# Kernel optimization log

Hardware: AMD Instinct MI355X
Metric: run time of the kernel (lower is better)

Reference implementation:

```python
import jax, jax.numpy as jnp
import numpy as np

B, T, E = 2, 2048, 1024
H = 16
D = E // H  # head_dim = 64


def setup_inputs() -> dict:
    key = jax.random.key(0)
    ks = jax.random.split(key, 9)
    s = 1.0 / np.sqrt(E)
    inp = {"x": jax.random.normal(ks[0], (B, T, E), dtype=jnp.float32)}
    # Linear params (torch nn.Linear: y = x @ W.T + b)
    inp["Wq"] = jax.random.uniform(ks[1], (E, E), jnp.float32, -s, s)
    inp["bq"] = jax.random.uniform(ks[2], (E,), jnp.float32, -s, s)
    inp["Wk"] = jax.random.uniform(ks[3], (E, E), jnp.float32, -s, s)
    inp["bk"] = jax.random.uniform(ks[4], (E,), jnp.float32, -s, s)
    inp["Wv"] = jax.random.uniform(ks[5], (E, E), jnp.float32, -s, s)
    inp["bv"] = jax.random.uniform(ks[6], (E,), jnp.float32, -s, s)
    inp["Wo"] = jax.random.uniform(ks[7], (E, E), jnp.float32, -s, s)
    inp["bo"] = jax.random.uniform(ks[8], (E,), jnp.float32, -s, s)
    return inp


def reference(x, Wq, bq, Wk, bk, Wv, bv, Wo, bo):
    # QKV projections, reshape to [B, H, T, D]
    def split_heads(y):
        return y.reshape(B, T, H, D).transpose(0, 2, 1, 3)

    Q = split_heads(x @ Wq.T + bq)
    K = split_heads(x @ Wk.T + bk)
    V = split_heads(x @ Wv.T + bv)

    scale = 1.0 / jnp.sqrt(jnp.asarray(D, x.dtype))
    scores = jnp.einsum("bhqd,bhkd->bhqk", Q, K) * scale  # [B,H,T,T]
    attn = jax.nn.softmax(scores, axis=-1)
    out = jnp.einsum("bhqk,bhkd->bhqd", attn, V)  # [B,H,T,D]
    out = out.transpose(0, 2, 1, 3).reshape(B, T, E)
    # dropout is identity in eval mode
    return out @ Wo.T + bo
```

## Files before the change

### kernel.cpp

```cpp
#include <hip/hip_runtime.h>
#include <math.h>

#define BB 2
#define TT 2048
#define EE 1024
#define HH 16
#define DD 64
#define MM (BB*TT)
#define KK EE

typedef short bf16x8 __attribute__((ext_vector_type(8)));
typedef float f32x4  __attribute__((ext_vector_type(4)));
typedef float f32x16 __attribute__((ext_vector_type(16)));
typedef unsigned int u32x4 __attribute__((ext_vector_type(4)));

__device__ __forceinline__ unsigned short f2bf(float f) {
  unsigned int u = __float_as_uint(f);
  u = (u + 0x7FFFu + ((u >> 16) & 1u)) >> 16;
  return (unsigned short)u;
}

__device__ __forceinline__ unsigned int cvtpk(float lo, float hi) {
  unsigned int r;
  asm("v_cvt_pk_bf16_f32 %0, %1, %2" : "=v"(r) : "v"(lo), "v"(hi));
  return r;
}

__device__ __forceinline__ void plswap(unsigned int &a, unsigned int &b) {
  asm("v_permlane32_swap_b32 %0, %1" : "+v"(a), "+v"(b));
}

__device__ __forceinline__ void async16(const void* g, void* l) {
  __builtin_amdgcn_global_load_lds(
      (const __attribute__((address_space(1))) unsigned int*)g,
      (__attribute__((address_space(3))) unsigned int*)l, 16, 0, 0);
}

__global__ __launch_bounds__(256) void to_bf16(
    const float* __restrict__ x,  const float* __restrict__ wq,
    const float* __restrict__ wk, const float* __restrict__ wv,
    const float* __restrict__ wo,
    unsigned short* __restrict__ xh, unsigned short* __restrict__ wcat,
    unsigned short* __restrict__ woh)
{
  int c = blockIdx.x * 256 + threadIdx.x;
  const float* src; unsigned short* dst; int off;
  if (c < 1048576) { src = x; dst = xh; off = c; }
  else {
    int r = c - 1048576;
    int w = r >> 18;
    off = r & 262143;
    if      (w == 0) { src = wq; dst = wcat; }
    else if (w == 1) { src = wk; dst = wcat + (1 << 20); }
    else if (w == 2) { src = wv; dst = wcat + (2 << 20); }
    else             { src = wo; dst = woh; }
  }
  float4 v = ((const float4*)src)[off];
  ushort4 h;
  h.x = f2bf(v.x); h.y = f2bf(v.y); h.z = f2bf(v.z); h.w = f2bf(v.w);
  ((ushort4*)dst)[off] = h;
}

template<int MODE>
__global__ __launch_bounds__(512, 6) void gemm_bf16(
    const unsigned short* __restrict__ A, const unsigned short* __restrict__ B,
    const float* __restrict__ b0p, const float* __restrict__ b1p,
    const float* __restrict__ b2p,
    unsigned short* __restrict__ oq, unsigned short* __restrict__ ok,
    unsigned short* __restrict__ ov, float* __restrict__ ofp, float qscale)
{
  constexpr int NT = (MODE == 0) ? 128 : 64;
  constexpr int JN = NT / 32;
  constexpr int BROWS = NT * 32;
  constexpr int TOT = (MODE == 0) ? 16 : 12;
  __shared__ unsigned short S[12288 + 3 * BROWS];

  const int tid  = threadIdx.x;
  const int lane = tid & 63;
  const int wv   = tid >> 6;
  const int col  = lane & 15;
  const int quad = lane >> 4;
  const int wm = (wv & 3) * 32;
  const int wn = (wv >> 2) * (NT / 2);
  const int m0 = blockIdx.x * 128;
  const int n0 = blockIdx.y * NT;

  const int srow = lane >> 2;
  const int sw16 = (((lane & 3) ^ ((lane >> 2) & 3) ^ (lane >> 4)) << 3);
  const int fswA = ((quad ^ (col & 3) ^ (col >> 2)) << 3);

  auto stage = [&](int kt, int slot) {
#pragma unroll
    for (int s = 0; s < 2; ++s) {
      const int t = wv * 2 + s;
      if (t < TOT) {
        const unsigned short* src; int rb, g0, loff;
        if (t < 8) { src = A; rb = t * 16;       g0 = m0; loff = slot * 4096; }
        else       { src = B; rb = (t - 8) * 16; g0 = n0; loff = 12288 + slot * BROWS; }
        async16(src + (size_t)(g0 + rb + srow) * KK + kt + sw16,
                S + loff + rb * 32);
      }
    }
  };

  f32x4 acc[2][JN];
  const f32x4 z = {0.f, 0.f, 0.f, 0.f};
#pragma unroll
  for (int i = 0; i < 2; ++i)
#pragma unroll
    for (int j = 0; j < JN; ++j) acc[i][j] = z;

  stage(0, 0);

#define GBODY(T, SL, S2, DOSTAGE, VMC) do {                                   \
    if (DOSTAGE) stage(((T) + 1) * 32, S2);                                   \
    asm volatile("s_waitcnt vmcnt(" #VMC ")" ::: "memory");                   \
    __builtin_amdgcn_sched_barrier(0);                                        \
    __builtin_amdgcn_s_barrier();                                             \
    __builtin_amdgcn_sched_barrier(0);                                        \
    const unsigned short* Asb = S + (SL) * 4096;                              \
    const unsigned short* Bsb = S + 12288 + (SL) * BROWS;                     \
    bf16x8 bfr[JN];                                                           \
    _Pragma("unroll")                                                         \
    for (int j = 0; j < JN; ++j)                                              \
      bfr[j] = *(const bf16x8*)(Bsb + (wn + j * 16 + col) * 32 + fswA);       \
    _Pragma("unroll")                                                         \
    for (int i = 0; i < 2; ++i) {                                             \
      bf16x8 af = *(const bf16x8*)(Asb + (wm + i * 16 + col) * 32 + fswA);    \
      _Pragma("unroll")                                                       \
      for (int j = 0; j < JN; ++j)                                            \
        acc[i][j] = __builtin_amdgcn_mfma_f32_16x16x32_bf16(af, bfr[j], acc[i][j], 0, 0, 0); \
    }                                                                         \
  } while (0)

  for (int t = 0; t < 30; t += 3) {
    GBODY(t + 0, 0, 1, 1, 2);
    GBODY(t + 1, 1, 2, 1, 2);
    GBODY(t + 2, 2, 0, 1, 2);
  }
  GBODY(30, 0, 1, 1, 2);
  GBODY(31, 1, 0, 0, 0);
#undef GBODY

  unsigned short* Cs = S;
  if (MODE == 0) {
    __syncthreads();
    const int region = n0 >> 10;
    const float* bias = (region == 0) ? b0p : (region == 1) ? b1p : b2p;
    const float scl = (region == 0) ? qscale : 1.0f;
    const int nlbase = n0 & 1023;
    const int h0 = nlbase >> 6;
    const int b = m0 >> 11, t0 = m0 & (TT - 1);
    if (region < 2) {
#pragma unroll
      for (int i = 0; i < 2; ++i)
#pragma unroll
        for (int j = 0; j < 4; ++j) {
          const int nt = wn + j * 16 + col;
          const float bs = bias[nlbase + nt];
#pragma unroll
          for (int r = 0; r < 4; ++r) {
            const int mt = wm + i * 16 + quad * 4 + r;
            Cs[mt * 136 + nt] = f2bf((acc[i][j][r] + bs) * scl);
          }
        }
      __syncthreads();
      unsigned short* dst = (region == 0) ? oq : ok;
#pragma unroll
      for (int s = 0; s < 4; ++s) {
        const int u = s * 512 + tid;
        const int mt = u >> 4, hs = (u >> 3) & 1, ch = u & 7;
        const size_t g = ((size_t)(b * HH + h0 + hs) * TT + t0 + mt) * DD + ch * 8;
        *(uint4*)(dst + g) = *(const uint4*)(Cs + mt * 136 + hs * 64 + ch * 8);
      }
    } else {
#pragma unroll
      for (int i = 0; i < 2; ++i)
#pragma unroll
        for (int j = 0; j < 4; ++j) {
          const int nt = wn + j * 16 + col;
          const float bs = bias[nlbase + nt];
          ushort4 pk;
          pk.x = f2bf(acc[i][j][0] + bs);
          pk.y = f2bf(acc[i][j][1] + bs);
          pk.z = f2bf(acc[i][j][2] + bs);
          pk.w = f2bf(acc[i][j][3] + bs);
          *(ushort4*)(Cs + nt * 136 + wm + i * 16 + quad * 4) = pk;
        }
      __syncthreads();
#pragma unroll
      for (int s = 0; s < 4; ++s) {
        const int u = s * 512 + tid;
        const int nt = u >> 4, ch = u & 15;
        const int d = nt & 63, hs = nt >> 6;
        const size_t g = ((size_t)(b * HH + h0 + hs) * DD + d) * TT + t0 + ch * 8;
        *(uint4*)(ov + g) = *(const uint4*)(Cs + nt * 136 + ch * 8);
      }
    }
  } else {
#pragma unroll
    for (int i = 0; i < 2; ++i) {
#pragma unroll
      for (int j = 0; j < JN; ++j) {
        const int n = n0 + wn + j * 16 + col;
        const float bs = b0p[n];
#pragma unroll
        for (int r = 0; r < 4; ++r) {
          const int m = m0 + wm + i * 16 + quad * 4 + r;
          ofp[(size_t)m * EE + n] = acc[i][j][r] + bs;
        }
      }
    }
  }
}

__global__ __launch_bounds__(512, 4) void flash_mfma(
    const unsigned short* __restrict__ Qb, const unsigned short* __restrict__ Kb,
    const unsigned short* __restrict__ Vtb, unsigned short* __restrict__ ctx)
{
  __shared__ unsigned short Qs[128 * 64];
  __shared__ unsigned short Ks[4][64 * 64];
  __shared__ unsigned short Vts[4][64 * 64];

  const int tid  = threadIdx.x;
  const int lane = tid & 63;
  const int wv   = tid >> 6;
  const int lq   = lane & 31;
  const int hf   = lane >> 5;
  const int wq   = wv & 3;
  const int wk2  = wv >> 2;
  const int gid  = blockIdx.x;
  const int bh   = gid & 31;
  const int q0   = (gid >> 5) * 128;

  const unsigned short* Qg = Qb  + (size_t)bh * TT * DD;
  const unsigned short* Kg = Kb  + (size_t)bh * TT * DD;
  const unsigned short* Vg = Vtb + (size_t)bh * DD * TT;

  const int srow = lane >> 3;
  const int swb  = ((lane & 7) ^ (lane >> 3)) << 3;

  const int rbK = wq * 16;
  const bool isK = (wv < 4);
  const int sw0 = swb ^ ((((rbK    ) >> 3) & 7) << 3);
  const int sw1 = swb ^ ((((rbK + 8) >> 3) & 7) << 3);
  const unsigned short* g0 =
      (isK ? Kg + (size_t)(rbK + srow) * DD : Vg + (size_t)(rbK + srow) * TT) + sw0;
  const unsigned short* g1 =
      (isK ? Kg + (size_t)(rbK + 8 + srow) * DD : Vg + (size_t)(rbK + 8 + srow) * TT) + sw1;
  unsigned short* l0 = (isK ? &Ks[0][0] : &Vts[0][0]) + rbK * 64;
  unsigned short* l1 = l0 + 8 * 64;
  const int gstep = isK ? 64 * DD : 64;

  auto stage_kv = [&](int ti, int slot) {
    const size_t go = (size_t)ti * gstep;
    async16(g0 + go, l0 + slot * 4096);
    async16(g1 + go, l1 + slot * 4096);
  };

  const int l7 = lane & 7;
  const int d3 = lq >> 3;
  int koff[4], voff[2][2];
#pragma unroll
  for (int s = 0; s < 4; ++s)
    koff[s] = ((wk2 * 32 + lq) * 64 +
               (((2 * s + hf) ^ l7 ^ ((wk2 * 4 + d3) & 7)) << 3)) * 2;
#pragma unroll
  for (int m = 0; m < 2; ++m)
#pragma unroll
    for (int sg = 0; sg < 2; ++sg)
      voff[m][sg] = ((m * 32 + lq) * 64 +
                     (((wk2 * 4 + 2 * sg + hf) ^ l7 ^ ((m * 4 + d3) & 7)) << 3)) * 2;

#pragma unroll
  for (int s = 0; s < 2; ++s) {
    const int rb = wv * 16 + s * 8;
    const int sq = swb ^ (((rb >> 3) & 7) << 3);
    async16(Qg + (size_t)(q0 + rb + srow) * DD + sq, &Qs[rb * 64]);
  }
  stage_kv(0, 0);
  stage_kv(1, 1);
  __syncthreads();

  bf16x8 aq[4];
#pragma unroll
  for (int s = 0; s < 4; ++s)
    aq[s] = *(const bf16x8*)(Qs + (wq * 32 + lq) * 64 +
                             (((2 * s + hf) ^ l7 ^ ((wq * 4 + d3) & 7)) << 3));

  const f32x16 z16 = {0.f,0.f,0.f,0.f,0.f,0.f,0.f,0.f,
                      0.f,0.f,0.f,0.f,0.f,0.f,0.f,0.f};
  f32x16 o_acc[2], sacc, nsacc;
  o_acc[0] = z16; o_acc[1] = z16;
  float lpart = 0.f;

  {
    const char* Kp = (const char*)&Ks[0][0];
    bf16x8 ak = *(const bf16x8*)(Kp + koff[0]);
    sacc = __builtin_amdgcn_mfma_f32_32x32x16_bf16(ak, aq[0], z16, 0, 0, 0);
#pragma unroll
    for (int s = 1; s < 4; ++s) {
      ak = *(const bf16x8*)(Kp + koff[s]);
      sacc = __builtin_amdgcn_mfma_f32_32x32x16_bf16(ak, aq[s], sacc, 0, 0, 0);
    }
  }

#define BODY(T, S0, S1, S2, DOSTAGE, DOQK, VMC, SIN, SOUT) do {               \
    if (DOSTAGE) stage_kv((T) + 2, S2);                                       \
    asm volatile("s_waitcnt vmcnt(" #VMC ")" ::: "memory");                   \
    __builtin_amdgcn_sched_barrier(0);                                        \
    __builtin_amdgcn_s_barrier();                                             \
    __builtin_amdgcn_sched_barrier(0);                                        \
    bf16x8 pa0, pa1;                                                          \
    {      \
      float e0 = __builtin_amdgcn_exp2f(SIN[0]);                              \
      float e1 = __builtin_amdgcn_exp2f(SIN[1]);                              \
      float e2 = __builtin_amdgcn_exp2f(SIN[2]);                              \
      float e3 = __builtin_amdgcn_exp2f(SIN[3]);                              \
      float e4 = __builtin_amdgcn_exp2f(SIN[4]);                              \
      float e5 = __builtin_amdgcn_exp2f(SIN[5]);                              \
      float e6 = __builtin_amdgcn_exp2f(SIN[6]);                              \
      float e7 = __builtin_amdgcn_exp2f(SIN[7]);                              \
      lpart += ((e0 + e1) + (e2 + e3)) + ((e4 + e5) + (e6 + e7));             \
      unsigned int a0 = cvtpk(e0, e1), b0 = cvtpk(e4, e5);                    \
      unsigned int a1 = cvtpk(e2, e3), b1 = cvtpk(e6, e7);                    \
      plswap(a0, b0); plswap(a1, b1);                                         \
      u32x4 w = {a0, a1, b0, b1};                                             \
      pa0 = __builtin_bit_cast(bf16x8, w);                                    \
    }                                                                         \
    {                                                     \
      float e0 = __builtin_amdgcn_exp2f(SIN[8]);                              \
      float e1 = __builtin_amdgcn_exp2f(SIN[9]);                              \
      float e2 = __builtin_amdgcn_exp2f(SIN[10]);                             \
      float e3 = __builtin_amdgcn_exp2f(SIN[11]);                             \
      float e4 = __builtin_amdgcn_exp2f(SIN[12]);                             \
      float e5 = __builtin_amdgcn_exp2f(SIN[13]);                             \
      float e6 = __builtin_amdgcn_exp2f(SIN[14]);                             \
      float e7 = __builtin_amdgcn_exp2f(SIN[15]);                             \
      lpart += ((e0 + e1) + (e2 + e3)) + ((e4 + e5) + (e6 + e7));             \
      unsigned int a0 = cvtpk(e0, e1), b0 = cvtpk(e4, e5);                    \
      unsigned int a1 = cvtpk(e2, e3), b1 = cvtpk(e6, e7);                    \
      plswap(a0, b0); plswap(a1, b1);                                         \
      u32x4 w = {a0, a1, b0, b1};                                             \
      pa1 = __builtin_bit_cast(bf16x8, w);                                    \
    }                                                                         \
    __builtin_amdgcn_s_setprio(1);                                            \
    if (DOQK) {     \
      const char* Kp = (const char*)&Ks[S1][0];                               \
      bf16x8 ak = *(const bf16x8*)(Kp + koff[0]);                             \
      SOUT = __builtin_amdgcn_mfma_f32_32x32x16_bf16(ak, aq[0], z16, 0, 0, 0);\
      _Pragma("unroll")                                                       \
      for (int s = 1; s < 4; ++s) {                                           \
        ak = *(const bf16x8*)(Kp + koff[s]);                                  \
        SOUT = __builtin_amdgcn_mfma_f32_32x32x16_bf16(ak, aq[s], SOUT, 0, 0, 0); \
      }                                                                       \
    }                                                                         \
    {                                                              \
      const char* Vp = (const char*)&Vts[S0][0];                              \
      _Pragma("unroll")                                                       \
      for (int m = 0; m < 2; ++m) {                                           \
        bf16x8 v0 = *(const bf16x8*)(Vp + voff[m][0]);                        \
        bf16x8 v1 = *(const bf16x8*)(Vp + voff[m][1]);                        \
        o_acc[m] = __builtin_amdgcn_mfma_f32_32x32x16_bf16(pa0, v0, o_acc[m], 0, 0, 0); \
        o_acc[m] = __builtin_amdgcn_mfma_f32_32x32x16_bf16(pa1, v1, o_acc[m], 0, 0, 0); \
      }                                                                       \
    }                                                                         \
    __builtin_amdgcn_s_setprio(0);                                            \
  } while (0)

  for (int t = 0; t < 28; t += 4) {
    BODY(t + 0, 0, 1, 2, 1, 1, 2, sacc, nsacc);
    BODY(t + 1, 1, 2, 3, 1, 1, 2, nsacc, sacc);
    BODY(t + 2, 2, 3, 0, 1, 1, 2, sacc, nsacc);
    BODY(t + 3, 3, 0, 1, 1, 1, 2, nsacc, sacc);
  }
  BODY(28, 0, 1, 2, 1, 1, 2, sacc, nsacc);
  BODY(29, 1, 2, 3, 1, 1, 2, nsacc, sacc);
  BODY(30, 2, 3, 0, 0, 1, 0, sacc, nsacc);
  BODY(31, 3, 0, 1, 0, 0, 0, nsacc, sacc);
#undef BODY

  float* Qf = (float*)&Qs[0];
  float* Of = (float*)&Ks[0][0];
  unsigned short* Cs = &Vts[0][0];
  const int bq = bh >> 4, head = bh & 15;

  float lw = lpart + __shfl_xor(lpart, 32);
  if (lane < 32) Qf[wv * 32 + lane] = lw;
  __syncthreads();

  if (wv >= 4) {
#pragma unroll
    for (int m = 0; m < 2; ++m)
#pragma unroll
      for (int r = 0; r < 16; ++r) {
        const int ql = (r & 3) + 8 * (r >> 2) + 4 * hf;
        Of[wq * 2048 + ql * 64 + m * 32 + lq] = o_acc[m][r];
      }
  }
  __syncthreads();

  if (wv < 4) {
    float linv[16];
#pragma unroll
    for (int r = 0; r < 16; ++r) {
      const int ql = (r & 3) + 8 * (r >> 2) + 4 * hf;
      linv[r] = 1.0f / (Qf[wv * 32 + ql] + Qf[(wv + 4) * 32 + ql]);
    }
#pragma unroll
    for (int m = 0; m < 2; ++m)
#pragma unroll
      for (int r = 0; r < 16; ++r) {
        const int ql = (r & 3) + 8 * (r >> 2) + 4 * hf;
        const float val =
            (o_acc[m][r] + Of[wq * 2048 + ql * 64 + m * 32 + lq]) * linv[r];
        const int row = wq * 32 + ql, d = m * 32 + lq;
        Cs[row * 64 + (((d >> 3) ^ (row & 7)) << 3) + (d & 7)] = f2bf(val);
      }
  }
  __syncthreads();

#pragma unroll
  for (int s = 0; s < 2; ++s) {
    const int u = s * 512 + tid;
    const int mr = u >> 3, ch = u & 7;
    const size_t g = ((size_t)(bq * TT + q0 + mr)) * EE + head * DD + ch * 8;
    const int chs = (ch ^ (mr & 7)) << 3;
    *(uint4*)(ctx + g) = *(const uint4*)(Cs + mr * 64 + chs);
  }
}

extern "C" void kernel_launch(void* const* d_in, const int* in_sizes, int n_in,
                              void* d_out, int out_size, void* d_ws, size_t ws_size,
                              hipStream_t stream) {
  const float* x  = (const float*)d_in[0];
  const float* Wq = (const float*)d_in[1];
  const float* bq = (const float*)d_in[2];
  const float* Wk = (const float*)d_in[3];
  const float* bk = (const float*)d_in[4];
  const float* Wv = (const float*)d_in[5];
  const float* bv = (const float*)d_in[6];
  const float* Wo = (const float*)d_in[7];
  const float* bo = (const float*)d_in[8];

  unsigned short* p = (unsigned short*)d_ws;
  const size_t XN = (size_t)MM * EE;
  const size_t WN = (size_t)EE * EE;
  unsigned short* x_h    = p;           p += XN;
  unsigned short* Wcat_h = p;           p += 3 * WN;
  unsigned short* Wo_h   = p;           p += WN;
  unsigned short* Qb     = p;           p += XN;
  unsigned short* Kb     = p;           p += XN;
  unsigned short* Vtb    = p;           p += XN;
  unsigned short* ctx_h  = x_h;

  to_bf16<<<8192, 256, 0, stream>>>(x, Wq, Wk, Wv, Wo, x_h, Wcat_h, Wo_h);

  const float qscale = 0.125f * 1.44269504088896f;

  gemm_bf16<0><<<dim3(MM / 128, 3 * EE / 128), 512, 0, stream>>>(
      x_h, Wcat_h, bq, bk, bv, Qb, Kb, Vtb, nullptr, qscale);

  flash_mfma<<<dim3((TT / 128) * BB * HH), 512, 0, stream>>>(Qb, Kb, Vtb, ctx_h);

  gemm_bf16<2><<<dim3(MM / 128, EE / 64), 512, 0, stream>>>(
      ctx_h, Wo_h, bo, nullptr, nullptr,
      nullptr, nullptr, nullptr, (float*)d_out, 1.0f);
}
```

Before: 184.3 us.

## Remap GEMM blocks for XCD locality and add dedicated output-projection kernel

The QKV GEMM now uses a 1D grid with a block index remap that spreads consecutive blocks across the 8 XCDs. The aim is to keep blocks that share A/B tiles in the same L2. The output projection moves to a new gemm_out kernel with the same remap, a 4-slot ring buffer, and two k-steps per barrier, which halves the barriers per k iteration. The cost is more code and some duplicated GEMM logic.

Measured after the change: 189.5 us. 1.03x slower.

```diff
diff --git a/kernel.cpp b/kernel.cpp
--- a/kernel.cpp
+++ b/kernel.cpp
@@ -69,10 +69,10 @@
     unsigned short* __restrict__ oq, unsigned short* __restrict__ ok,
     unsigned short* __restrict__ ov, float* __restrict__ ofp, float qscale)
 {
-  constexpr int NT = (MODE == 0) ? 128 : 64;
-  constexpr int JN = NT / 32;
+  constexpr int NT = 128;
+  constexpr int JN = 4;
   constexpr int BROWS = NT * 32;
-  constexpr int TOT = (MODE == 0) ? 16 : 12;
+  constexpr int TOT = 16;
   __shared__ unsigned short S[12288 + 3 * BROWS];
 
   const int tid  = threadIdx.x;
@@ -82,8 +82,10 @@
   const int quad = lane >> 4;
   const int wm = (wv & 3) * 32;
   const int wn = (wv >> 2) * (NT / 2);
-  const int m0 = blockIdx.x * 128;
-  const int n0 = blockIdx.y * NT;
+  const int lin = blockIdx.x;
+  const int v   = (lin & 7) * 96 + (lin >> 3);
+  const int m0 = (v & 31) * 128;
+  const int n0 = (v >> 5) * 128;
 
   const int srow = lane >> 2;
   const int sw16 = (((lane & 3) ^ ((lane >> 2) & 3) ^ (lane >> 4)) << 3);
@@ -143,7 +145,7 @@
 #undef GBODY
 
   unsigned short* Cs = S;
-  if (MODE == 0) {
+  {
     __syncthreads();
     const int region = n0 >> 10;
     const float* bias = (region == 0) ? b0p : (region == 1) ? b1p : b2p;
@@ -197,18 +199,97 @@
         *(uint4*)(ov + g) = *(const uint4*)(Cs + nt * 136 + ch * 8);
       }
     }
-  } else {
-#pragma unroll
-    for (int i = 0; i < 2; ++i) {
-#pragma unroll
-      for (int j = 0; j < JN; ++j) {
-        const int n = n0 + wn + j * 16 + col;
-        const float bs = b0p[n];
-#pragma unroll
-        for (int r = 0; r < 4; ++r) {
-          const int m = m0 + wm + i * 16 + quad * 4 + r;
-          ofp[(size_t)m * EE + n] = acc[i][j][r] + bs;
-        }
+  }
+}
+
+__global__ __launch_bounds__(512, 6) void gemm_out(
+    const unsigned short* __restrict__ A, const unsigned short* __restrict__ B,
+    const float* __restrict__ bias, float* __restrict__ ofp)
+{
+  __shared__ unsigned short S[24576];
+
+  const int tid  = threadIdx.x;
+  const int lane = tid & 63;
+  const int wv   = tid >> 6;
+  const int col  = lane & 15;
+  const int quad = lane >> 4;
+  const int wm = (wv & 3) * 32;
+  const int wn = (wv >> 2) * 32;
+  const int lin = blockIdx.x;
+  const int v   = (lin & 7) * 64 + (lin >> 3);
+  const int m0 = (v & 31) * 128;
+  const int n0 = (v >> 5) * 64;
+
+  const int srow = lane >> 2;
+  const int sw16 = (((lane & 3) ^ ((lane >> 2) & 3) ^ (lane >> 4)) << 3);
+  const int fswA = ((quad ^ (col & 3) ^ (col >> 2)) << 3);
+
+  auto stage = [&](int kt, int slot) {
+#pragma unroll
+    for (int s = 0; s < 2; ++s) {
+      const int t = wv * 2 + s;
+      if (t < 12) {
+        const unsigned short* src; int rb, g0, loff;
+        if (t < 8) { src = A; rb = t * 16;       g0 = m0; loff = slot * 4096; }
+        else       { src = B; rb = (t - 8) * 16; g0 = n0; loff = 16384 + slot * 2048; }
+        async16(src + (size_t)(g0 + rb + srow) * KK + kt + sw16,
+                S + loff + rb * 32);
+      }
+    }
+  };
+
+  f32x4 acc[2][2];
+  const f32x4 z = {0.f, 0.f, 0.f, 0.f};
+#pragma unroll
+  for (int i = 0; i < 2; ++i)
+#pragma unroll
+    for (int j = 0; j < 2; ++j) acc[i][j] = z;
+
+  stage(0, 0);
+  stage(32, 1);
+
+#define GCOMP(SL) do {                                                        \
+    const unsigned short* Asb = S + (SL) * 4096;                              \
+    const unsigned short* Bsb = S + 16384 + (SL) * 2048;                      \
+    bf16x8 b0 = *(const bf16x8*)(Bsb + (wn + col) * 32 + fswA);               \
+    bf16x8 b1 = *(const bf16x8*)(Bsb + (wn + 16 + col) * 32 + fswA);          \
+    _Pragma("unroll")                                                         \
+    for (int i = 0; i < 2; ++i) {                                             \
+      bf16x8 af = *(const bf16x8*)(Asb + (wm + i * 16 + col) * 32 + fswA);    \
+      acc[i][0] = __builtin_amdgcn_mfma_f32_16x16x32_bf16(af, b0, acc[i][0], 0, 0, 0); \
+      acc[i][1] = __builtin_amdgcn_mfma_f32_16x16x32_bf16(af, b1, acc[i][1], 0, 0, 0); \
+    }                                                                         \
+} while (0)
+
+#define REGION2(T, SLa, SLb, SSa, SSb, DOSTAGE, VMC) do {                     \
+    asm volatile("s_waitcnt vmcnt(" #VMC ")" ::: "memory");                   \
+    __builtin_amdgcn_sched_barrier(0);                                        \
+    __builtin_amdgcn_s_barrier();                                             \
+    __builtin_amdgcn_sched_barrier(0);                                        \
+    if (DOSTAGE) { stage(((T) + 2) * 32, SSa); stage(((T) + 3) * 32, SSb); }  \
+    GCOMP(SLa);                                                               \
+    GCOMP(SLb);                                                               \
+} while (0)
+
+  for (int t = 0; t < 28; t += 4) {
+    REGION2(t + 0, 0, 1, 2, 3, 1, 0);
+    REGION2(t + 2, 2, 3, 0, 1, 1, 0);
+  }
+  REGION2(28, 0, 1, 2, 3, 1, 0);
+  REGION2(30, 2, 3, 0, 1, 0, 0);
+#undef REGION2
+#undef GCOMP
+
+#pragma unroll
+  for (int i = 0; i < 2; ++i) {
+#pragma unroll
+    for (int j = 0; j < 2; ++j) {
+      const int n = n0 + wn + j * 16 + col;
+      const float bs = bias[n];
+#pragma unroll
+      for (int r = 0; r < 4; ++r) {
+        const int m = m0 + wm + i * 16 + quad * 4 + r;
+        ofp[(size_t)m * EE + n] = acc[i][j][r] + bs;
       }
     }
   }
@@ -454,16 +535,14 @@
   unsigned short* Vtb    = p;           p += XN;
   unsigned short* ctx_h  = x_h;
 
+  const float qscale = 0.125f * 1.44269504088896f;
+
   to_bf16<<<8192, 256, 0, stream>>>(x, Wq, Wk, Wv, Wo, x_h, Wcat_h, Wo_h);
 
-  const float qscale = 0.125f * 1.44269504088896f;
-
-  gemm_bf16<0><<<dim3(MM / 128, 3 * EE / 128), 512, 0, stream>>>(
+  gemm_bf16<0><<<dim3(768), 512, 0, stream>>>(
       x_h, Wcat_h, bq, bk, bv, Qb, Kb, Vtb, nullptr, qscale);
 
   flash_mfma<<<dim3((TT / 128) * BB * HH), 512, 0, stream>>>(Qb, Kb, Vtb, ctx_h);
 
-  gemm_bf16<2><<<dim3(MM / 128, EE / 64), 512, 0, stream>>>(
-      ctx_h, Wo_h, bo, nullptr, nullptr,
-      nullptr, nullptr, nullptr, (float*)d_out, 1.0f);
-}
+  gemm_out<<<dim3(512), 512, 0, stream>>>(ctx_h, Wo_h, bo, (float*)d_out);
+}
```
